# Optimization experiments

Hardware: AMD Instinct MI355X
Metric: run time of the kernel (lower is better)

## Reference

```python
import jax, jax.numpy as jnp
import numpy as np

NUM_CLASSES = 19
LOSS_WEIGHT = 0.5
EPS_MEAN = 1e-6   # added to per-class pixel counts
EPS_PD = 1e-6     # torch F.pairwise_distance eps (added to the difference)


def setup_inputs() -> dict:
    key = jax.random.key(0)
    k1, k2, k3 = jax.random.split(key, 3)
    N, C, H, W = 8, 19, 512, 1024
    preds_S = jax.random.normal(k1, (N, C, H, W), dtype=jnp.float32)
    preds_T = jax.random.normal(k2, (N, C, H, W), dtype=jnp.float32)
    gt = jax.random.randint(k3, (N, 1, H, W), 0, NUM_CLASSES, dtype=jnp.int32)
    return {"preds_S": preds_S, "preds_T": preds_T, "gt": gt}


def _class_means(feats, labels, counts_inv):
    # feats: [N, HW, C], labels: [N, HW] int, counts_inv: [N, K]
    seg = jax.vmap(lambda x, s: jax.ops.segment_sum(x, s, num_segments=NUM_CLASSES))
    sums = seg(feats, labels)                      # [N, K, C]
    return sums * counts_inv[..., None]            # [N, K, C]


def reference(preds_S, preds_T, gt):
    N, C, H, W = preds_S.shape
    # gt: F.interpolate(gt.float(), [H,W], bilinear, align_corners=False).int()
    gt_f = jax.image.resize(gt.astype(jnp.float32), (N, 1, H, W), method="bilinear")
    labels = gt_f.astype(jnp.int32).reshape(N, H * W)            # [N, HW]

    # per-class counts (shared between S and T since masks are identical)
    ones = jnp.ones((N, H * W), dtype=jnp.float32)
    seg1 = jax.vmap(lambda x, s: jax.ops.segment_sum(x, s, num_segments=NUM_CLASSES))
    counts = seg1(ones, labels)                                   # [N, K]
    counts_inv = 1.0 / (counts + EPS_MEAN)

    xs = jnp.transpose(preds_S.reshape(N, C, H * W), (0, 2, 1))   # [N, HW, C]
    xt = jnp.transpose(preds_T.reshape(N, C, H * W), (0, 2, 1))
    v_S = _class_means(xs, labels, counts_inv)                    # [N, K, C]
    v_T = _class_means(xt, labels, counts_inv)

    # pairwise euclidean distances between class prototypes (torch eps on diff)
    d_S = v_S[:, :, None, :] - v_S[:, None, :, :] + EPS_PD        # [N, K, K, C]
    d_T = v_T[:, :, None, :] - v_T[:, None, :, :] + EPS_PD
    e_S = jnp.sqrt(jnp.sum(d_S * d_S, axis=-1))                   # [N, K, K]
    e_T = jnp.sqrt(jnp.sum(d_T * d_T, axis=-1))

    tri = jnp.triu(jnp.ones((NUM_CLASSES, NUM_CLASSES), dtype=jnp.float32), k=1)
    per_pair = 0.5 * (e_T - e_S) ** 2                             # [N, K, K]
    loss = jnp.mean(jnp.sum(per_pair * tri, axis=(1, 2)))         # mean over batch
    return LOSS_WEIGHT * loss
```

## Files before the change

### kernel.cpp

```cpp
#include <hip/hip_runtime.h>

#define NCLS 19
#define HWSZ (512*1024)
#define NB   8
#define CHUNK 2048
#define TPX   256
#define NT    (CHUNK/TPX)
#define EPSM  1e-6f
#define EPSPD 1e-6f

#define ROWP 20
#define COLP 32
#define SUMS_ELEMS (NB*2*ROWP*COLP)
#define F4T  (NCLS*TPX/4)

typedef short bf16x8 __attribute__((ext_vector_type(8)));
typedef float f32x16 __attribute__((ext_vector_type(16)));

__device__ __forceinline__ short bfh(float v) {
    return (short)(__builtin_bit_cast(unsigned, v) >> 16);
}
__device__ __forceinline__ short bfl(float v) {
    unsigned u = __builtin_bit_cast(unsigned, v);
    float lf = v - __builtin_bit_cast(float, u & 0xFFFF0000u);
    return (short)(__builtin_bit_cast(unsigned, lf) >> 16);
}

#define STAGE_DECL(j) float4 sreg##j, treg##j; long off##j; int lds##j;

#define STAGE_INIT(j) {                                                     \
    int f = tid + (j) * 256; if ((j) == 4 && f >= F4T) f = F4T - 1;         \
    const int row_ = f >> 6, g_ = f & 63;                                   \
    off##j = ((long)(n * NCLS + row_)) * HWSZ + chunk0 + g_ * 4;            \
    lds##j = row_ * 64 + (g_ ^ (row_ & 7)); }

#define STAGE_LOAD(j, tt) {                                                 \
    const long o_ = off##j + (long)(tt) * TPX;                              \
    sreg##j = *(const float4*)(S + o_);                                     \
    treg##j = *(const float4*)(T + o_); }

#define STAGE_WRITE(j)                                                      \
    if ((j) < 4 || tid + (j) * 256 < F4T) {                                 \
        ((float4*)Sb)[lds##j] = sreg##j;                                    \
        ((float4*)Tb)[lds##j] = treg##j; }

__global__ __launch_bounds__(256, 3) void icl_sums(
    const float* __restrict__ S, const float* __restrict__ T,
    const int* __restrict__ gt, float* __restrict__ sums)
{
    __shared__ float Sb[NCLS * TPX];
    __shared__ float Tb[NCLS * TPX];
    __shared__ int   lab[CHUNK];
    __shared__ float red[2][ROWP][COLP];

    const int tid = threadIdx.x;
    const int n   = blockIdx.y;
    const long chunk0 = (long)blockIdx.x * CHUNK;

    for (int i = tid; i < 2 * ROWP * COLP; i += 256) ((float*)red)[i] = 0.f;

    const int4* gp = (const int4*)(gt + (long)n * HWSZ + chunk0);
    ((int4*)lab)[tid]       = gp[tid];
    ((int4*)lab)[tid + 256] = gp[tid + 256];

    const int wave = tid >> 6;
    const int lane = tid & 63;
    const int r    = lane & 31;
    const int kg   = lane >> 5;
    const bool isT = wave >= 2;
    const int  ph  = wave & 1;

    STAGE_DECL(0) STAGE_DECL(1) STAGE_DECL(2) STAGE_DECL(3) STAGE_DECL(4)
    STAGE_INIT(0) STAGE_INIT(1) STAGE_INIT(2) STAGE_INIT(3) STAGE_INIT(4)

    f32x16 acc = {0,0,0,0,0,0,0,0,0,0,0,0,0,0,0,0};
    const bf16x8 ones = {0x3F80,0x3F80,0x3F80,0x3F80,0x3F80,0x3F80,0x3F80,0x3F80};

    const float* xb = isT ? Tb : Sb;
    const float* zb = (const float*)red;

    STAGE_LOAD(0, 0) STAGE_LOAD(1, 0) STAGE_LOAD(2, 0) STAGE_LOAD(3, 0) STAGE_LOAD(4, 0)

    for (int t = 0; t < NT; ++t) {
        if (t > 0) __syncthreads();
        STAGE_WRITE(0) STAGE_WRITE(1) STAGE_WRITE(2) STAGE_WRITE(3) STAGE_WRITE(4)
        __syncthreads();
        if (t + 1 < NT) {
            STAGE_LOAD(0, t + 1) STAGE_LOAD(1, t + 1) STAGE_LOAD(2, t + 1)
            STAGE_LOAD(3, t + 1) STAGE_LOAD(4, t + 1)
        }

#pragma unroll
        for (int st = 0; st < 8; ++st) {
            const int px = ph * 128 + st * 16 + kg * 8;

            const int4 l0 = *(const int4*)&lab[t * TPX + px];
            const int4 l1 = *(const int4*)&lab[t * TPX + px + 4];
            bf16x8 B;
            B[0] = (l0.x == r) ? (short)0x3F80 : (short)0;
            B[1] = (l0.y == r) ? (short)0x3F80 : (short)0;
            B[2] = (l0.z == r) ? (short)0x3F80 : (short)0;
            B[3] = (l0.w == r) ? (short)0x3F80 : (short)0;
            B[4] = (l1.x == r) ? (short)0x3F80 : (short)0;
            B[5] = (l1.y == r) ? (short)0x3F80 : (short)0;
            B[6] = (l1.z == r) ? (short)0x3F80 : (short)0;
            B[7] = (l1.w == r) ? (short)0x3F80 : (short)0;

            const int go  = px >> 2;
            const int gr0 = go ^ (r & 7);
            const int gr1 = (go + 1) ^ (r & 7);
            const float4* f4 = (const float4*)((r < NCLS) ? (xb + r * TPX) : zb);
            const float4 d0 = f4[gr0];
            const float4 d1 = f4[gr1];

            bf16x8 hi, lo;
            hi[0]=bfh(d0.x); lo[0]=bfl(d0.x);  hi[1]=bfh(d0.y); lo[1]=bfl(d0.y);
            hi[2]=bfh(d0.z); lo[2]=bfl(d0.z);  hi[3]=bfh(d0.w); lo[3]=bfl(d0.w);
            hi[4]=bfh(d1.x); lo[4]=bfl(d1.x);  hi[5]=bfh(d1.y); lo[5]=bfl(d1.y);
            hi[6]=bfh(d1.z); lo[6]=bfl(d1.z);  hi[7]=bfh(d1.w); lo[7]=bfl(d1.w);

            if (r == NCLS && !isT) hi = ones;

            acc = __builtin_amdgcn_mfma_f32_32x32x16_bf16(hi, B, acc, 0, 0, 0);
            acc = __builtin_amdgcn_mfma_f32_32x32x16_bf16(lo, B, acc, 0, 0, 0);
        }
    }

#pragma unroll
    for (int e = 0; e < 16; ++e) {
        const int row = (e & 3) + 8 * (e >> 2) + 4 * kg;
        if (row < ROWP) atomicAdd(&red[isT ? 1 : 0][row][r], acc[e]);
    }
    __syncthreads();

    float* gs = sums + (long)n * 2 * ROWP * COLP;
    for (int i = tid; i < 2 * ROWP * COLP; i += 256) {
        if ((i & 31) < NCLS) atomicAdd(&gs[i], ((const float*)red)[i]);
    }
}

__global__ __launch_bounds__(256) void icl_final(
    const float* __restrict__ sums, float* __restrict__ out)
{
    __shared__ float v[NB][2][NCLS][NCLS];
    __shared__ float red2[256];
    const int tid = threadIdx.x;

    for (int i = tid; i < NB * 2 * NCLS * NCLS; i += 256) {
        const int c = i % NCLS;
        const int k = (i / NCLS) % NCLS;
        const int t = (i / (NCLS * NCLS)) % 2;
        const int n = i / (2 * NCLS * NCLS);
        const float cnt = sums[((n * 2 + 0) * ROWP + NCLS) * COLP + k];
        const float val = sums[((n * 2 + t) * ROWP + c) * COLP + k];
        v[n][t][k][c] = val * (1.f / (cnt + EPSM));
    }
    __syncthreads();

    float acc = 0.f;
    const int NPAIR = NCLS * (NCLS - 1) / 2;
    for (int i = tid; i < NB * NPAIR; i += 256) {
        const int n = i / NPAIR;
        int rem = i % NPAIR;
        int k1 = 0;
        while (rem >= NCLS - 1 - k1) { rem -= NCLS - 1 - k1; ++k1; }
        const int k2 = k1 + 1 + rem;
        float ss = 0.f, st = 0.f;
#pragma unroll
        for (int c = 0; c < NCLS; ++c) {
            const float ds = v[n][0][k1][c] - v[n][0][k2][c] + EPSPD;
            const float dt = v[n][1][k1][c] - v[n][1][k2][c] + EPSPD;
            ss = fmaf(ds, ds, ss);
            st = fmaf(dt, dt, st);
        }
        const float e = sqrtf(st) - sqrtf(ss);
        acc += 0.5f * e * e;
    }

    red2[tid] = acc;
    __syncthreads();
    for (int s = 128; s > 0; s >>= 1) {
        if (tid < s) red2[tid] += red2[tid + s];
        __syncthreads();
    }
    if (tid == 0) out[0] = 0.5f * red2[0] / (float)NB;
}

extern "C" void kernel_launch(void* const* d_in, const int* in_sizes, int n_in,
                              void* d_out, int out_size, void* d_ws, size_t ws_size,
                              hipStream_t stream) {
    const float* S  = (const float*)d_in[0];
    const float* T  = (const float*)d_in[1];
    const int*   gt = (const int*)d_in[2];

    float* sums = (float*)d_ws;
    hipMemsetAsync(d_ws, 0, SUMS_ELEMS * sizeof(float), stream);

    dim3 grid(HWSZ / CHUNK, NB);
    icl_sums<<<grid, 256, 0, stream>>>(S, T, gt, sums);
    icl_final<<<1, 256, 0, stream>>>(sums, (float*)d_out);
}
```

Before: 157.4 us.

## Double-buffer global prefetch, pack labels to bytes, and relayout LDS tiles

Global loads are now prefetched two tiles ahead using two register sets, with the tile loop fully unrolled. Labels are packed to bytes in LDS, and the S/T tiles use a new swizzled float4 layout so each lane reads contiguous per-class vectors. Row 19 is filled with ones so the count path no longer needs a per-iteration branch, and the bf16 hi/lo split uses perm instructions. The aim is to hide global load latency and cut LDS and ALU work per MFMA, at the cost of much higher register pressure under the occupancy target of 3 blocks.

```diff
diff --git a/kernel.cpp b/kernel.cpp
--- a/kernel.cpp
+++ b/kernel.cpp
@@ -16,41 +16,73 @@
 
 typedef short bf16x8 __attribute__((ext_vector_type(8)));
 typedef float f32x16 __attribute__((ext_vector_type(16)));
-
-__device__ __forceinline__ short bfh(float v) {
-    return (short)(__builtin_bit_cast(unsigned, v) >> 16);
-}
-__device__ __forceinline__ short bfl(float v) {
-    unsigned u = __builtin_bit_cast(unsigned, v);
-    float lf = v - __builtin_bit_cast(float, u & 0xFFFF0000u);
-    return (short)(__builtin_bit_cast(unsigned, lf) >> 16);
-}
-
-#define STAGE_DECL(j) float4 sreg##j, treg##j; long off##j; int lds##j;
-
-#define STAGE_INIT(j) {                                                     \
-    int f = tid + (j) * 256; if ((j) == 4 && f >= F4T) f = F4T - 1;         \
-    const int row_ = f >> 6, g_ = f & 63;                                   \
-    off##j = ((long)(n * NCLS + row_)) * HWSZ + chunk0 + g_ * 4;            \
-    lds##j = row_ * 64 + (g_ ^ (row_ & 7)); }
-
-#define STAGE_LOAD(j, tt) {                                                 \
-    const long o_ = off##j + (long)(tt) * TPX;                              \
-    sreg##j = *(const float4*)(S + o_);                                     \
-    treg##j = *(const float4*)(T + o_); }
-
-#define STAGE_WRITE(j)                                                      \
-    if ((j) < 4 || tid + (j) * 256 < F4T) {                                 \
-        ((float4*)Sb)[lds##j] = sreg##j;                                    \
-        ((float4*)Tb)[lds##j] = treg##j; }
+typedef unsigned uint4v __attribute__((ext_vector_type(4)));
+
+#define SG_DECL(set) float4 s##set##0, s##set##1, s##set##2, s##set##3, s##set##4, \
+                            t##set##0, t##set##1, t##set##2, t##set##3, t##set##4;
+
+#define SG_INIT(j) { int f = tid + (j)*256; if ((j) == 4 && f >= F4T) f = F4T - 1; \
+    const int row_ = f >> 6, g_ = f & 63;                                          \
+    const int blk_ = ((g_ >> 2) << 1) | (g_ & 1);                   \
+    const int slot_ = (((g_ >> 1) & 1) * 20) + row_;                \
+    widx##j = blk_ * 40 + (slot_ ^ (blk_ & 7));                                     \
+    goff##j = ((long)(n * NCLS + row_)) * HWSZ + chunk0 + (g_ << 2); }
+
+#define SG_LOAD(set, j, tt) { const long o_ = goff##j + (long)(tt) * TPX; \
+    s##set##j = *(const float4*)(S + o_);                                 \
+    t##set##j = *(const float4*)(T + o_); }
+
+#define SG_LOADS(set, tt) SG_LOAD(set,0,tt) SG_LOAD(set,1,tt) SG_LOAD(set,2,tt) \
+                          SG_LOAD(set,3,tt) SG_LOAD(set,4,tt)
+
+#define SG_WRITE(set, j) { Sb4[widx##j] = s##set##j; Tb4[widx##j] = t##set##j; }
+#define SG_WRITES(set) SG_WRITE(set,0) SG_WRITE(set,1) SG_WRITE(set,2) \
+                       SG_WRITE(set,3) SG_WRITE(set,4)
+
+#define CVT(pA, pB, HI, LO) {                                                      \
+    const unsigned uA = __builtin_bit_cast(unsigned, pA);                          \
+    const unsigned uB = __builtin_bit_cast(unsigned, pB);                          \
+    HI = __builtin_amdgcn_perm(uB, uA, 0x07060302u);                               \
+    const float fa = (pA) - __builtin_bit_cast(float, uA & 0xFFFF0000u);           \
+    const float fb = (pB) - __builtin_bit_cast(float, uB & 0xFFFF0000u);           \
+    LO = __builtin_amdgcn_perm(__builtin_bit_cast(unsigned, fb),                   \
+                               __builtin_bit_cast(unsigned, fa), 0x07060302u); }
+
+#define BBIT(word, sh, ei) { const unsigned lb_ = ((word) >> (sh)) & 255u;         \
+    B[ei] = (lb_ == ur) ? (short)0x3F80 : (short)0; }
+
+#define COMPUTE_TILE(t_) {                                                          \
+    _Pragma("unroll")                                                               \
+    for (int i = 0; i < 8; ++i) {                                                   \
+        const uint2 pk = *(const uint2*)(labP + (t_) * 256 + i * 16);               \
+        const float4 d0 = xb4[ra[(2*i) & 7]     + (2*i) * 40];                      \
+        const float4 d1 = xb4[ra[(2*i+1) & 7]   + (2*i+1) * 40];                    \
+        bf16x8 B;                                                                   \
+        BBIT(pk.x, 0, 0) BBIT(pk.x, 8, 1) BBIT(pk.x, 16, 2) BBIT(pk.x, 24, 3)      \
+        BBIT(pk.y, 0, 4) BBIT(pk.y, 8, 5) BBIT(pk.y, 16, 6) BBIT(pk.y, 24, 7)      \
+        unsigned h0, h1, h2, h3, l0_, l1_, l2_, l3_;                                \
+        CVT(d0.x, d0.y, h0, l0_)  CVT(d0.z, d0.w, h1, l1_)                          \
+        CVT(d1.x, d1.y, h2, l2_)  CVT(d1.z, d1.w, h3, l3_)                          \
+        const bf16x8 hi = __builtin_bit_cast(bf16x8, (uint4v){h0, h1, h2, h3});     \
+        const bf16x8 lo = __builtin_bit_cast(bf16x8, (uint4v){l0_, l1_, l2_, l3_}); \
+        acc = __builtin_amdgcn_mfma_f32_32x32x16_bf16(hi, B, acc, 0, 0, 0);         \
+        acc = __builtin_amdgcn_mfma_f32_32x32x16_bf16(lo, B, acc, 0, 0, 0);         \
+    } }
+
+#define TILE(set, t_) {                                                             \
+    if ((t_) > 0) __syncthreads();                                                  \
+    SG_WRITES(set)                                                                  \
+    __syncthreads();                                                                \
+    if ((t_) + 2 < NT) { SG_LOADS(set, (t_) + 2) }                                  \
+    COMPUTE_TILE(t_) }
 
 __global__ __launch_bounds__(256, 3) void icl_sums(
     const float* __restrict__ S, const float* __restrict__ T,
     const int* __restrict__ gt, float* __restrict__ sums)
 {
-    __shared__ float Sb[NCLS * TPX];
-    __shared__ float Tb[NCLS * TPX];
-    __shared__ int   lab[CHUNK];
+    __shared__ float4 Sb4[32 * 40];
+    __shared__ float4 Tb4[32 * 40];
+    __shared__ unsigned char labU[CHUNK];
     __shared__ float red[2][ROWP][COLP];
 
     const int tid = threadIdx.x;
@@ -59,72 +91,50 @@
 
     for (int i = tid; i < 2 * ROWP * COLP; i += 256) ((float*)red)[i] = 0.f;
 
-    const int4* gp = (const int4*)(gt + (long)n * HWSZ + chunk0);
-    ((int4*)lab)[tid]       = gp[tid];
-    ((int4*)lab)[tid + 256] = gp[tid + 256];
-
-    const int wave = tid >> 6;
-    const int lane = tid & 63;
-    const int r    = lane & 31;
-    const int kg   = lane >> 5;
+    if (tid < 128) {
+        const int b = tid >> 2, kg_ = (tid >> 1) & 1, tb = tid & 1;
+        const int idx = b * 40 + (((kg_ * 20) + 19) ^ (b & 7));
+        (tb ? Tb4 : Sb4)[idx] = make_float4(1.f, 1.f, 1.f, 1.f);
+    }
+
+    {
+        const int4* gp = (const int4*)(gt + (long)n * HWSZ + chunk0);
+        const int4 a = gp[tid], b = gp[tid + 256];
+        const unsigned p0 = (unsigned)a.x | ((unsigned)a.y << 8) |
+                            ((unsigned)a.z << 16) | ((unsigned)a.w << 24);
+        const unsigned p1 = (unsigned)b.x | ((unsigned)b.y << 8) |
+                            ((unsigned)b.z << 16) | ((unsigned)b.w << 24);
+        ((unsigned*)labU)[tid]       = p0;
+        ((unsigned*)labU)[tid + 256] = p1;
+    }
+
+    int widx0, widx1, widx2, widx3, widx4;
+    long goff0, goff1, goff2, goff3, goff4;
+    SG_INIT(0) SG_INIT(1) SG_INIT(2) SG_INIT(3) SG_INIT(4)
+    SG_DECL(A) SG_DECL(B)
+
+    const int wave = tid >> 6, lane = tid & 63;
+    const int r  = lane & 31;
+    const int kg = lane >> 5;
     const bool isT = wave >= 2;
     const int  ph  = wave & 1;
-
-    STAGE_DECL(0) STAGE_DECL(1) STAGE_DECL(2) STAGE_DECL(3) STAGE_DECL(4)
-    STAGE_INIT(0) STAGE_INIT(1) STAGE_INIT(2) STAGE_INIT(3) STAGE_INIT(4)
+    const unsigned ur = (unsigned)r;
+
+    const int sbase = kg * 20 + (r < 20 ? r : r - 12);
+    int ra[8];
+#pragma unroll
+    for (int k = 0; k < 8; ++k) ra[k] = ph * 640 + (sbase ^ k);
+
+    const float4* xb4 = isT ? Tb4 : Sb4;
+    const unsigned char* labP = labU + ph * 128 + kg * 8;
 
     f32x16 acc = {0,0,0,0,0,0,0,0,0,0,0,0,0,0,0,0};
-    const bf16x8 ones = {0x3F80,0x3F80,0x3F80,0x3F80,0x3F80,0x3F80,0x3F80,0x3F80};
-
-    const float* xb = isT ? Tb : Sb;
-    const float* zb = (const float*)red;
-
-    STAGE_LOAD(0, 0) STAGE_LOAD(1, 0) STAGE_LOAD(2, 0) STAGE_LOAD(3, 0) STAGE_LOAD(4, 0)
-
-    for (int t = 0; t < NT; ++t) {
-        if (t > 0) __syncthreads();
-        STAGE_WRITE(0) STAGE_WRITE(1) STAGE_WRITE(2) STAGE_WRITE(3) STAGE_WRITE(4)
-        __syncthreads();
-        if (t + 1 < NT) {
-            STAGE_LOAD(0, t + 1) STAGE_LOAD(1, t + 1) STAGE_LOAD(2, t + 1)
-            STAGE_LOAD(3, t + 1) STAGE_LOAD(4, t + 1)
-        }
-
-#pragma unroll
-        for (int st = 0; st < 8; ++st) {
-            const int px = ph * 128 + st * 16 + kg * 8;
-
-            const int4 l0 = *(const int4*)&lab[t * TPX + px];
-            const int4 l1 = *(const int4*)&lab[t * TPX + px + 4];
-            bf16x8 B;
-            B[0] = (l0.x == r) ? (short)0x3F80 : (short)0;
-            B[1] = (l0.y == r) ? (short)0x3F80 : (short)0;
-            B[2] = (l0.z == r) ? (short)0x3F80 : (short)0;
-            B[3] = (l0.w == r) ? (short)0x3F80 : (short)0;
-            B[4] = (l1.x == r) ? (short)0x3F80 : (short)0;
-            B[5] = (l1.y == r) ? (short)0x3F80 : (short)0;
-            B[6] = (l1.z == r) ? (short)0x3F80 : (short)0;
-            B[7] = (l1.w == r) ? (short)0x3F80 : (short)0;
-
-            const int go  = px >> 2;
-            const int gr0 = go ^ (r & 7);
-            const int gr1 = (go + 1) ^ (r & 7);
-            const float4* f4 = (const float4*)((r < NCLS) ? (xb + r * TPX) : zb);
-            const float4 d0 = f4[gr0];
-            const float4 d1 = f4[gr1];
-
-            bf16x8 hi, lo;
-            hi[0]=bfh(d0.x); lo[0]=bfl(d0.x);  hi[1]=bfh(d0.y); lo[1]=bfl(d0.y);
-            hi[2]=bfh(d0.z); lo[2]=bfl(d0.z);  hi[3]=bfh(d0.w); lo[3]=bfl(d0.w);
-            hi[4]=bfh(d1.x); lo[4]=bfl(d1.x);  hi[5]=bfh(d1.y); lo[5]=bfl(d1.y);
-            hi[6]=bfh(d1.z); lo[6]=bfl(d1.z);  hi[7]=bfh(d1.w); lo[7]=bfl(d1.w);
-
-            if (r == NCLS && !isT) hi = ones;
-
-            acc = __builtin_amdgcn_mfma_f32_32x32x16_bf16(hi, B, acc, 0, 0, 0);
-            acc = __builtin_amdgcn_mfma_f32_32x32x16_bf16(lo, B, acc, 0, 0, 0);
-        }
-    }
+
+    SG_LOADS(A, 0)
+    SG_LOADS(B, 1)
+
+    TILE(A, 0) TILE(B, 1) TILE(A, 2) TILE(B, 3)
+    TILE(A, 4) TILE(B, 5) TILE(A, 6) TILE(B, 7)
 
 #pragma unroll
     for (int e = 0; e < 16; ++e) {
```

After: 152.2 us. 3.3% less time.
